# Optimization experiments

Measured on AMD Instinct MI355X. Metric: run time of the kernel, lower is better.

## Reference

```python
import jax, jax.numpy as jnp
import numpy as np

B, N, FIN, F = 512, 512, 2, 128  # batch, n_sites, input features, hidden features


def setup_inputs() -> dict:
    key = jax.random.key(0)
    k1, k2 = jax.random.split(key)
    inputs = jax.random.normal(k1, (B, N, FIN), dtype=jnp.float32)
    # LSTM dense kernel over concat([inputs_i, hidden]) -> 4*F gates (i, f, g, o)
    Wk = jax.random.normal(k2, (FIN + F, 4 * F), dtype=jnp.float32) / np.sqrt(FIN + F)
    b = jnp.zeros((4 * F,), dtype=jnp.float32)
    return {"inputs": inputs, "Wk": Wk, "b": b}


def reference(inputs, Wk, b):
    # exclusive=True, reorder_idx=None: inputs_i = 0 at k=0, else inputs[:, k-1, :];
    # memory state = outputs[:, k-1, :] = previous hidden (zeros buffer at k=0).
    batch = inputs.shape[0]
    x_shift = jnp.concatenate(
        [jnp.zeros_like(inputs[:, :1, :]), inputs[:, :-1, :]], axis=1
    )  # (B, N, FIN)
    xs = jnp.swapaxes(x_shift, 0, 1)  # (N, B, FIN) scan over sites

    c0 = jnp.zeros((batch, F), dtype=inputs.dtype)
    h0 = jnp.zeros((batch, F), dtype=inputs.dtype)

    def step(carry, x_t):
        c, h = carry
        ifgo = jnp.concatenate([x_t, h], axis=-1) @ Wk + b  # (B, 4F)
        i, f, g, o = jnp.split(ifgo, 4, axis=-1)
        c = jax.nn.sigmoid(f) * c + jax.nn.sigmoid(i) * jnp.tanh(g)
        h = jax.nn.sigmoid(o) * jnp.tanh(c)
        return (c, h), h

    _, hs = jax.lax.scan(step, (c0, h0), xs)  # hs: (N, B, F)
    outputs = jnp.swapaxes(hs, 0, 1)  # (B, N, F)
    return outputs
```

## Files before the change

kernel.cpp:

```cpp
#include <hip/hip_runtime.h>

#define B_   512
#define N_   512
#define FIN_ 2
#define F_   128
#define G_   512
#define XSTRIDE 1040
#define HSTRIDE 160

typedef _Float16 half8  __attribute__((ext_vector_type(8)));
typedef float    float4_ __attribute__((ext_vector_type(4)));
typedef float    float2_ __attribute__((ext_vector_type(2)));

#define LOG2E_  1.44269504f
#define LOG2E2_ 2.88539008f

__device__ __forceinline__ float sigmoid_(float x) {
    return __builtin_amdgcn_rcpf(1.f + __builtin_amdgcn_exp2f(-LOG2E_ * x));
}

__device__ __forceinline__ void lstm_step(
    const _Float16* hsrc,
    _Float16* hdst,
    float* outp,
    const half8 (&wf)[4][4], const float (&w0r)[4], const float (&w1r)[4],
    const float (&br)[4], float4_ (&acc)[4], float2_ xv,
    float& cs, int grp)
{
    half8 af[4];
#pragma unroll
    for (int s2 = 0; s2 < 4; ++s2)
        af[s2] = *reinterpret_cast<const half8*>(hsrc + s2 * 32 + grp * 8);

#pragma unroll
    for (int t = 0; t < 4; ++t)
        acc[t][0] = fmaf(xv[0], w0r[t], fmaf(xv[1], w1r[t], br[t]));

#pragma unroll
    for (int s2 = 0; s2 < 4; ++s2)
#pragma unroll
        for (int t = 0; t < 4; ++t)
            acc[t] = __builtin_amdgcn_mfma_f32_16x16x32_f16(af[s2], wf[t][s2], acc[t], 0, 0, 0);

    const float gi = sigmoid_(acc[0][0]);
    const float gf = sigmoid_(acc[1][0]);
    const float rg = __builtin_amdgcn_rcpf(1.f + __builtin_amdgcn_exp2f(LOG2E2_ * acc[2][0]));
    const float gg = fmaf(-2.f, rg, 1.f);
    const float go = sigmoid_(acc[3][0]);
    cs = fmaf(gf, cs, gi * gg);
    const float rc = __builtin_amdgcn_rcpf(1.f + __builtin_amdgcn_exp2f(LOG2E2_ * cs));
    const float h = fmaf(-2.f * go, rc, go);
    *hdst = (_Float16)h;
    *outp = h;
    asm volatile("s_waitcnt lgkmcnt(0)\n\ts_barrier" ::: "memory");
}

__global__ void __launch_bounds__(512)
lstm_scan(const float* __restrict__ inp, const float* __restrict__ Wk,
          const float* __restrict__ bias, float* __restrict__ out)
{
    const int bb   = blockIdx.x;
    const int tid  = threadIdx.x;
    const int w    = tid >> 6;
    const int lane = tid & 63;
    const int c15  = lane & 15;
    const int grp  = lane >> 4;

    __shared__ __align__(64) _Float16 h_lds[2][2 * HSTRIDE];
    __shared__ __align__(64) float    x_lds[2 * XSTRIDE];

    half8 wf[4][4];
    float w0r[4], w1r[4], br[4];
#pragma unroll
    for (int t = 0; t < 4; ++t) {
        const int col = t * F_ + w * 16 + c15;
        w0r[t] = Wk[col];
        w1r[t] = Wk[G_ + col];
        br[t]  = bias[col];
#pragma unroll
        for (int s2 = 0; s2 < 4; ++s2) {
            half8 f;
#pragma unroll
            for (int e = 0; e < 8; ++e)
                f[e] = (_Float16)Wk[(size_t)(2 + s2 * 32 + grp * 8 + e) * G_ + col];
            wf[t][s2] = f;
        }
    }

    {
        const float* xsrc = inp + (size_t)(2 * bb) * (N_ * FIN_);
        const int i4 = tid * 4;
        float4_ v = *reinterpret_cast<const float4_*>(xsrc + i4);
        const int row = i4 >> 10, idx = i4 & 1023;
        *reinterpret_cast<float4_*>(&x_lds[row * XSTRIDE + idx]) = v;
    }
    for (int i = tid; i < 2 * 2 * HSTRIDE; i += 512)
        ((_Float16*)h_lds)[i] = (_Float16)0.f;
    __syncthreads();

    const int r    = (lane >> 4) & 1;
    const int hrow = (c15 >> 2) & 1;

    const _Float16* hr0 = &h_lds[0][hrow * HSTRIDE];
    const _Float16* hr1 = &h_lds[1][hrow * HSTRIDE];
    _Float16* hw0 = &h_lds[0][r * HSTRIDE + w * 16 + c15];
    _Float16* hw1 = &h_lds[1][r * HSTRIDE + w * 16 + c15];
    const float* xq = &x_lds[r * XSTRIDE];
    float* outp = out + (size_t)(2 * bb + r) * N_ * F_ + w * 16 + c15;

    float cs = 0.f;
    float4_ acc[4];
#pragma unroll
    for (int t = 0; t < 4; ++t) { acc[t][0] = 0.f; acc[t][1] = 0.f; acc[t][2] = 0.f; acc[t][3] = 0.f; }

    float2_ xz; xz[0] = 0.f; xz[1] = 0.f;

    lstm_step(hr0, hw1, outp, wf, w0r, w1r, br, acc, xz, cs, grp);
    outp += F_;

    float2_ x1 = *reinterpret_cast<const float2_*>(xq + 0);
    float2_ x2 = *reinterpret_cast<const float2_*>(xq + 2);

    for (int i = 0; i < 255; ++i) {
        const float2_ xn1 = *reinterpret_cast<const float2_*>(xq + 4 * i + 4);
        const float2_ xn2 = *reinterpret_cast<const float2_*>(xq + 4 * i + 6);
        lstm_step(hr1, hw0, outp, wf, w0r, w1r, br, acc, x1, cs, grp);
        outp += F_;
        lstm_step(hr0, hw1, outp, wf, w0r, w1r, br, acc, x2, cs, grp);
        outp += F_;
        x1 = xn1; x2 = xn2;
    }
    lstm_step(hr1, hw0, outp, wf, w0r, w1r, br, acc, x1, cs, grp);
}

extern "C" void kernel_launch(void* const* d_in, const int* in_sizes, int n_in,
                              void* d_out, int out_size, void* d_ws, size_t ws_size,
                              hipStream_t stream) {
    const float* inp  = (const float*)d_in[0];
    const float* Wk   = (const float*)d_in[1];
    const float* bias = (const float*)d_in[2];
    float* out        = (float*)d_out;
    lstm_scan<<<dim3(B_ / 2), dim3(512), 0, stream>>>(inp, Wk, bias, out);
}
```

Measured before the change: 231.7 us.

## Rotate K-chunk order per wave, reorder MFMAs and gate math, move x prefetch into step

Each wave group now reads its h fragments in a rotated K order (XOR offset), with matching weight permutation, to spread LDS bank accesses across waves. The last MFMA round is reordered so the g, i and f gate accumulators finish before the o gate. The exp and rcp calls are interleaved to expose more independent transcendental work. The x prefetch is issued inside the step after the h loads rather than before it. All of this targets latency on the serial recurrence critical path, at the cost of more complex indexing and a reliance on the compiler keeping the intended instruction order.

```diff
diff --git a/kernel.cpp b/kernel.cpp
--- a/kernel.cpp
+++ b/kernel.cpp
@@ -15,41 +15,53 @@
 #define LOG2E_  1.44269504f
 #define LOG2E2_ 2.88539008f
 
-__device__ __forceinline__ float sigmoid_(float x) {
-    return __builtin_amdgcn_rcpf(1.f + __builtin_amdgcn_exp2f(-LOG2E_ * x));
-}
-
+template<bool PF>
 __device__ __forceinline__ void lstm_step(
     const _Float16* hsrc,
     _Float16* hdst,
     float* outp,
     const half8 (&wf)[4][4], const float (&w0r)[4], const float (&w1r)[4],
     const float (&br)[4], float4_ (&acc)[4], float2_ xv,
-    float& cs, int grp)
+    float& cs, int grp, int rotofs,
+    const float* xpf, float2_& pf1, float2_& pf2)
 {
     half8 af[4];
 #pragma unroll
-    for (int s2 = 0; s2 < 4; ++s2)
-        af[s2] = *reinterpret_cast<const half8*>(hsrc + s2 * 32 + grp * 8);
+    for (int i = 0; i < 4; ++i)
+        af[i] = *reinterpret_cast<const half8*>(hsrc + ((i * 32) ^ rotofs) + grp * 8);
+
+    if (PF) {
+        pf1 = *reinterpret_cast<const float2_*>(xpf);
+        pf2 = *reinterpret_cast<const float2_*>(xpf + 2);
+    }
 
 #pragma unroll
     for (int t = 0; t < 4; ++t)
         acc[t][0] = fmaf(xv[0], w0r[t], fmaf(xv[1], w1r[t], br[t]));
 
 #pragma unroll
-    for (int s2 = 0; s2 < 4; ++s2)
+    for (int i = 0; i < 3; ++i)
 #pragma unroll
         for (int t = 0; t < 4; ++t)
-            acc[t] = __builtin_amdgcn_mfma_f32_16x16x32_f16(af[s2], wf[t][s2], acc[t], 0, 0, 0);
+            acc[t] = __builtin_amdgcn_mfma_f32_16x16x32_f16(af[i], wf[t][i], acc[t], 0, 0, 0);
+    acc[2] = __builtin_amdgcn_mfma_f32_16x16x32_f16(af[3], wf[2][3], acc[2], 0, 0, 0);
+    acc[0] = __builtin_amdgcn_mfma_f32_16x16x32_f16(af[3], wf[0][3], acc[0], 0, 0, 0);
+    acc[1] = __builtin_amdgcn_mfma_f32_16x16x32_f16(af[3], wf[1][3], acc[1], 0, 0, 0);
+    acc[3] = __builtin_amdgcn_mfma_f32_16x16x32_f16(af[3], wf[3][3], acc[3], 0, 0, 0);
 
-    const float gi = sigmoid_(acc[0][0]);
-    const float gf = sigmoid_(acc[1][0]);
-    const float rg = __builtin_amdgcn_rcpf(1.f + __builtin_amdgcn_exp2f(LOG2E2_ * acc[2][0]));
+    const float eg = __builtin_amdgcn_exp2f(LOG2E2_ * acc[2][0]);
+    const float ei = __builtin_amdgcn_exp2f(-LOG2E_ * acc[0][0]);
+    const float ef = __builtin_amdgcn_exp2f(-LOG2E_ * acc[1][0]);
+    const float rg = __builtin_amdgcn_rcpf(1.f + eg);
+    const float ri = __builtin_amdgcn_rcpf(1.f + ei);
+    const float rf = __builtin_amdgcn_rcpf(1.f + ef);
     const float gg = fmaf(-2.f, rg, 1.f);
-    const float go = sigmoid_(acc[3][0]);
-    cs = fmaf(gf, cs, gi * gg);
-    const float rc = __builtin_amdgcn_rcpf(1.f + __builtin_amdgcn_exp2f(LOG2E2_ * cs));
-    const float h = fmaf(-2.f * go, rc, go);
+    cs = fmaf(rf, cs, ri * gg);
+    const float eo = __builtin_amdgcn_exp2f(-LOG2E_ * acc[3][0]);
+    const float ec = __builtin_amdgcn_exp2f(LOG2E2_ * cs);
+    const float ro = __builtin_amdgcn_rcpf(1.f + eo);
+    const float rc = __builtin_amdgcn_rcpf(1.f + ec);
+    const float h = fmaf(-2.f * ro, rc, ro);
     *hdst = (_Float16)h;
     *outp = h;
     asm volatile("s_waitcnt lgkmcnt(0)\n\ts_barrier" ::: "memory");
@@ -65,6 +77,7 @@
     const int lane = tid & 63;
     const int c15  = lane & 15;
     const int grp  = lane >> 4;
+    const int rotofs = ((((w >> 2) ^ w) & 1) != 0) ? 64 : 0;
 
     __shared__ __align__(64) _Float16 h_lds[2][2 * HSTRIDE];
     __shared__ __align__(64) float    x_lds[2 * XSTRIDE];
@@ -78,12 +91,12 @@
         w1r[t] = Wk[G_ + col];
         br[t]  = bias[col];
 #pragma unroll
-        for (int s2 = 0; s2 < 4; ++s2) {
+        for (int i = 0; i < 4; ++i) {
             half8 f;
 #pragma unroll
             for (int e = 0; e < 8; ++e)
-                f[e] = (_Float16)Wk[(size_t)(2 + s2 * 32 + grp * 8 + e) * G_ + col];
-            wf[t][s2] = f;
+                f[e] = (_Float16)Wk[(size_t)(2 + ((i * 32) ^ rotofs) + grp * 8 + e) * G_ + col];
+            wf[t][i] = f;
         }
     }
 
@@ -114,23 +127,24 @@
     for (int t = 0; t < 4; ++t) { acc[t][0] = 0.f; acc[t][1] = 0.f; acc[t][2] = 0.f; acc[t][3] = 0.f; }
 
     float2_ xz; xz[0] = 0.f; xz[1] = 0.f;
+    float2_ pf1, pf2;
 
-    lstm_step(hr0, hw1, outp, wf, w0r, w1r, br, acc, xz, cs, grp);
+    lstm_step<true>(hr0, hw1, outp, wf, w0r, w1r, br, acc, xz, cs, grp, rotofs,
+                    xq, pf1, pf2);
     outp += F_;
 
-    float2_ x1 = *reinterpret_cast<const float2_*>(xq + 0);
-    float2_ x2 = *reinterpret_cast<const float2_*>(xq + 2);
-
     for (int i = 0; i < 255; ++i) {
-        const float2_ xn1 = *reinterpret_cast<const float2_*>(xq + 4 * i + 4);
-        const float2_ xn2 = *reinterpret_cast<const float2_*>(xq + 4 * i + 6);
-        lstm_step(hr1, hw0, outp, wf, w0r, w1r, br, acc, x1, cs, grp);
+        const float2_ xv1 = pf1;
+        const float2_ xv2 = pf2;
+        lstm_step<true>(hr1, hw0, outp, wf, w0r, w1r, br, acc, xv1, cs, grp,
+                        rotofs, xq + 4 * i + 4, pf1, pf2);
         outp += F_;
-        lstm_step(hr0, hw1, outp, wf, w0r, w1r, br, acc, x2, cs, grp);
+        lstm_step<false>(hr0, hw1, outp, wf, w0r, w1r, br, acc, xv2, cs, grp,
+                         rotofs, nullptr, pf1, pf2);
         outp += F_;
-        x1 = xn1; x2 = xn2;
     }
-    lstm_step(hr1, hw0, outp, wf, w0r, w1r, br, acc, x1, cs, grp);
+    lstm_step<false>(hr1, hw0, outp, wf, w0r, w1r, br, acc, pf1, cs, grp,
+                     rotofs, nullptr, pf1, pf2);
 }
 
 extern "C" void kernel_launch(void* const* d_in, const int* in_sizes, int n_in,
```

After: 234.6 us. About the same (+1.2%).
